# Performance work log

Measured on AMD Instinct MI355X. Metric: run time of the kernel, lower is better.

## Reference

```python
import jax, jax.numpy as jnp
import numpy as np
import math

B, P = 64, 2048
E_DRUG, E_PATH = 512, 512
ATTN_DIM, H, DEPTH = 1024, 8, 1
HD = ATTN_DIM // (2 * H)          # head_dim = 64
SCALING = HD ** (-0.5)
LAMBDA_INIT = 0.8 - 0.6 * math.exp(-0.3 * DEPTH)
EPS_SM = 1e-20
EPS_RMS = 1e-5


def stable_softmax(x, eps=EPS_SM):
    x = x.astype(jnp.float32)
    x = x - jnp.max(x, axis=-1, keepdims=True)
    ex = jnp.exp(x)
    return ex / (jnp.sum(ex, axis=-1, keepdims=True) + eps)


def setup_inputs() -> dict:
    key = jax.random.key(0)
    ks = jax.random.split(key, 11)
    d = 2 * H * HD  # = ATTN_DIM
    return {
        "query": jax.random.normal(ks[0], (B, 1, E_DRUG), jnp.float32),
        "key": jax.random.normal(ks[1], (B, P, E_PATH), jnp.float32),
        # Linear weights stored [in, out] (transpose of torch storage; same math)
        "Wq": jax.random.normal(ks[2], (E_DRUG, d), jnp.float32) * 0.02,
        "Wk": jax.random.normal(ks[3], (E_PATH, d), jnp.float32) * 0.02,
        "Wv": jax.random.normal(ks[4], (E_PATH, d), jnp.float32) * 0.02,
        "Wo": jax.random.normal(ks[5], (d, E_DRUG), jnp.float32) * 0.02,
        "lambda_q1": jax.random.normal(ks[6], (HD,), jnp.float32) * 0.1,
        "lambda_k1": jax.random.normal(ks[7], (HD,), jnp.float32) * 0.1,
        "lambda_q2": jax.random.normal(ks[8], (HD,), jnp.float32) * 0.1,
        "lambda_k2": jax.random.normal(ks[9], (HD,), jnp.float32) * 0.1,
        "rms_weight": jnp.ones((2 * HD,), jnp.float32),
    }


def reference(query, key, Wq, Wk, Wv, Wo,
              lambda_q1, lambda_k1, lambda_q2, lambda_k2, rms_weight):
    # Q: [B,1,H,2,HD] -> [B,H,2,1,HD]; K,V: [B,P,H,2,HD] -> [B,H,2,P,HD]
    Q = (query @ Wq).reshape(B, 1, H, 2, HD).transpose(0, 2, 3, 1, 4) * SCALING
    K = (key @ Wk).reshape(B, P, H, 2, HD).transpose(0, 2, 3, 1, 4)
    V = (key @ Wv).reshape(B, P, H, 2, HD)

    # scores: [B,H,2,1,P]
    scores = jnp.einsum('bhsqd,bhskd->bhsqk', Q, K)
    scores = stable_softmax(scores)

    lam1 = jnp.exp(jnp.sum(lambda_q1 * lambda_k1))
    lam2 = jnp.exp(jnp.sum(lambda_q2 * lambda_k2))
    lam = lam1 - lam2 + LAMBDA_INIT

    diff_attn = scores[:, :, 0] - lam * scores[:, :, 1]  # [B,H,1,P]

    V_cat = V.transpose(0, 2, 1, 3, 4).reshape(B, H, P, 2 * HD)  # [B,H,P,2HD]
    out = jnp.einsum('bhqp,bhpd->bhqd', diff_attn, V_cat)        # [B,H,1,2HD]

    # RMSNorm over last dim, affine
    var = jnp.mean(out * out, axis=-1, keepdims=True)
    out = out * jax.lax.rsqrt(var + EPS_RMS) * rms_weight
    out = out * (1.0 - LAMBDA_INIT)

    out = out.transpose(0, 2, 1, 3).reshape(B, 1, 2 * H * HD)
    out = out @ Wo  # [B,1,E_DRUG]
    return out, diff_attn
```

## Files before the change

kernel.cpp:

```cpp
#include <hip/hip_runtime.h>
#include <hip/hip_bf16.h>
#include <math.h>

#define B_ 64
#define P_ 2048
#define E_ 512
#define H_ 8
#define D_ 1024
#define NC_ 32
#define NG_ 4
#define SMEM_FUSED (65536 + 8704 + 2304 + 64 + 64)

#define BAR() do { asm volatile("s_waitcnt lgkmcnt(0)" ::: "memory"); \
                   __builtin_amdgcn_s_barrier(); } while (0)

static constexpr float SCALING_C = 0.125f;
static constexpr float LAMBDA_INIT_C = 0.35550906759096966f;

typedef float f32x4 __attribute__((ext_vector_type(4)));
typedef float f32x2 __attribute__((ext_vector_type(2)));
typedef short bf16x8 __attribute__((ext_vector_type(8)));

static __device__ __forceinline__ short f2bf(float f) {
    unsigned u = __builtin_bit_cast(unsigned, f);
    unsigned r = (u + 0x7fffu + ((u >> 16) & 1u)) >> 16;
    return (short)r;
}

__global__ __launch_bounds__(256) void k_qproj(const float* __restrict__ query,
                                               const float* __restrict__ Wq,
                                               const float* __restrict__ Wk,
                                               unsigned short* __restrict__ qkfrag) {
    int x = blockIdx.x, b = blockIdx.y, t = threadIdx.x;
    __shared__ float q[E_];
    __shared__ float qh[256];
    q[t] = query[b * E_ + t];
    q[t + 256] = query[b * E_ + t + 256];
    __syncthreads();
    {
        int j = x * 256 + t;
        const float* w = Wq + j;
        float s0 = 0.f, s1 = 0.f, s2 = 0.f, s3 = 0.f;
        #pragma unroll 4
        for (int e = 0; e < E_; e += 4) {
            s0 += q[e]     * w[(long)e * D_];
            s1 += q[e + 1] * w[(long)(e + 1) * D_];
            s2 += q[e + 2] * w[(long)(e + 2) * D_];
            s3 += q[e + 3] * w[(long)(e + 3) * D_];
        }
        qh[t] = ((s0 + s1) + (s2 + s3)) * SCALING_C;
    }
    __syncthreads();
    int hs_loc = t >> 6, l = t & 63;
    int hs = x * 4 + hs_loc;
    int e0 = l * 8;
    const float* qp = qh + hs_loc * 64;
    float acc[8];
    #pragma unroll
    for (int jj = 0; jj < 8; ++jj) {
        const f32x4* w = (const f32x4*)(Wk + (long)(e0 + jj) * D_ + hs * 64);
        float s = 0.f;
        #pragma unroll
        for (int d4 = 0; d4 < 16; ++d4) {
            f32x4 wv = w[d4];
            s += qp[d4 * 4 + 0] * wv[0] + qp[d4 * 4 + 1] * wv[1]
               + qp[d4 * 4 + 2] * wv[2] + qp[d4 * 4 + 3] * wv[3];
        }
        acc[jj] = s;
    }
    bf16x8 v;
    #pragma unroll
    for (int jj = 0; jj < 8; ++jj) v[jj] = f2bf(acc[jj]);
    *(bf16x8*)(qkfrag + (((long)b * 16 + (l >> 2)) * 64 + (l & 3) * 16 + hs) * 8) = v;
}

__global__ __launch_bounds__(512, 2) void k_fusedp(const float* __restrict__ key,
                                                   const unsigned short* __restrict__ qkfrag,
                                                   float* __restrict__ wexp,
                                                   float* __restrict__ ms, float* __restrict__ zs,
                                                   float* __restrict__ apart) {
    extern __shared__ __align__(16) char smem[];
    unsigned short* kswz = (unsigned short*)smem;
    float* scr           = (float*)(smem + 65536);
    unsigned short* wbf  = (unsigned short*)(smem + 74240);
    float* fac_l         = (float*)(smem + 76544);
    float* mrun_l        = (float*)(smem + 76608);

    int pcg = blockIdx.x, b = blockIdx.y;
    int t = threadIdx.x, wv = t >> 6, l = t & 63;
    int rt = wv >> 1, eh = wv & 1;
    int prow = rt * 16 + (l & 15);
    int xorv = ((prow & 7) << 3) ^ ((prow & 8) << 1);
    int ebase = eh * 256 + (l >> 4) * 8;

    if (t < 16) mrun_l[t] = -3.0e38f;

    bf16x8 qfr[8];
    {
        const bf16x8* qf = (const bf16x8*)(qkfrag + (long)b * 16 * 64 * 8);
        #pragma unroll
        for (int s = 0; s < 8; ++s) qfr[s] = qf[(eh * 8 + s) * 64 + l];
    }

    const float* kp = key + ((long)b * P_ + pcg * 512 + prow) * E_ + ebase;

    f32x4 x[16];
    #pragma unroll
    for (int s = 0; s < 8; ++s) {
        x[2 * s]     = *(const f32x4*)(kp + s * 32);
        x[2 * s + 1] = *(const f32x4*)(kp + s * 32 + 4);
    }

    f32x4 accp[4];
    #pragma unroll
    for (int i = 0; i < 4; ++i) accp[i] = {0.f, 0.f, 0.f, 0.f};

    for (int c = 0; c < 8; ++c) {
        {
            f32x4 acc = {0.f, 0.f, 0.f, 0.f};
            #pragma unroll
            for (int s = 0; s < 8; ++s) {
                f32x4 x0 = x[2 * s], x1 = x[2 * s + 1];
                bf16x8 a;
                a[0] = f2bf(x0[0]); a[1] = f2bf(x0[1]); a[2] = f2bf(x0[2]); a[3] = f2bf(x0[3]);
                a[4] = f2bf(x1[0]); a[5] = f2bf(x1[1]); a[6] = f2bf(x1[2]); a[7] = f2bf(x1[3]);
                *(bf16x8*)(kswz + prow * 512 + ((ebase + s * 32) ^ xorv)) = a;
                acc = __builtin_amdgcn_mfma_f32_16x16x32_bf16(a, qfr[s], acc, 0, 0, 0);
            }
            #pragma unroll
            for (int r = 0; r < 4; ++r)
                scr[eh * 1088 + (l & 15) * 68 + rt * 16 + (l >> 4) * 4 + r] = acc[r];
        }
        if (c < 7) {
            const float* kpn = kp + (long)(c + 1) * 64 * E_;
            #pragma unroll
            for (int s = 0; s < 8; ++s) {
                x[2 * s]     = *(const f32x4*)(kpn + s * 32);
                x[2 * s + 1] = *(const f32x4*)(kpn + s * 32 + 4);
            }
        }
        BAR();

        {
            int hs = t >> 5, i = t & 31;
            const float* s0p = scr + hs * 68 + i * 2;
            const float* s1p = s0p + 1088;
            float v0 = s0p[0] + s1p[0];
            float v1 = s0p[1] + s1p[1];
            float m = fmaxf(v0, v1);
            #pragma unroll
            for (int o = 16; o > 0; o >>= 1) m = fmaxf(m, __shfl_xor(m, o));
            float e0v = expf(v0 - m), e1v = expf(v1 - m);
            float z = e0v + e1v;
            #pragma unroll
            for (int o = 16; o > 0; o >>= 1) z += __shfl_xor(z, o);
            float mold = mrun_l[hs];
            float mnew = fmaxf(mold, m);
            float wsc = expf(m - mnew);
            if (i == 0) {
                mrun_l[hs] = mnew;
                fac_l[hs] = expf(mold - mnew);
                ms[((long)(pcg * 8 + c) * B_ + b) * 16 + hs] = m;
                zs[((long)(pcg * 8 + c) * B_ + b) * 16 + hs] = z;
            }
            f32x2 wv2; wv2[0] = e0v; wv2[1] = e1v;
            *(f32x2*)(wexp + ((long)b * 16 + hs) * P_ + pcg * 512 + c * 64 + i * 2) = wv2;
            unsigned lo = (unsigned short)f2bf(e0v * wsc);
            unsigned hi = (unsigned short)f2bf(e1v * wsc);
            *(unsigned*)(wbf + hs * 72 + i * 2) = lo | (hi << 16);
        }
        BAR();

        {
            f32x4 frv;
            frv[0] = fac_l[(l >> 4) * 4 + 0];
            frv[1] = fac_l[(l >> 4) * 4 + 1];
            frv[2] = fac_l[(l >> 4) * 4 + 2];
            frv[3] = fac_l[(l >> 4) * 4 + 3];
            const unsigned short* wrow = wbf + (l & 15) * 72;
            #pragma unroll
            for (int tile = 0; tile < 4; ++tile) {
                accp[tile] = accp[tile] * frv;
                int e = wv * 64 + tile * 16 + (l & 15);
                #pragma unroll
                for (int ks = 0; ks < 2; ++ks) {
                    int pbase = ks * 32 + (l >> 4) * 8;
                    bf16x8 af = *(const bf16x8*)(wrow + pbase);
                    int x2 = (pbase & 8) << 1;
                    bf16x8 bfv;
                    #pragma unroll
                    for (int j = 0; j < 8; ++j)
                        bfv[j] = (short)kswz[(pbase + j) * 512 + (e ^ (j << 3) ^ x2)];
                    accp[tile] = __builtin_amdgcn_mfma_f32_16x16x32_bf16(af, bfv, accp[tile], 0, 0, 0);
                }
            }
        }
        BAR();
    }

    {
        long abase = ((long)pcg * B_ + b) * 16 * E_;
        #pragma unroll
        for (int tile = 0; tile < 4; ++tile) {
            int e = wv * 64 + tile * 16 + (l & 15);
            #pragma unroll
            for (int r = 0; r < 4; ++r)
                apart[abase + (long)((l >> 4) * 4 + r) * E_ + e] = accp[tile][r];
        }
    }
}

__global__ __launch_bounds__(256) void k_comb(const float* __restrict__ wexp,
                                              const float* __restrict__ ms, const float* __restrict__ zs,
                                              const float* __restrict__ apart,
                                              const float* __restrict__ lq1, const float* __restrict__ lk1,
                                              const float* __restrict__ lq2, const float* __restrict__ lk2,
                                              const float* __restrict__ Wv, const float* __restrict__ rmsw,
                                              float* __restrict__ out1, float* __restrict__ on) {
    int h = blockIdx.x, b = blockIdx.y, t = threadIdx.x;
    __shared__ float lam_s;
    __shared__ float mc0s[NC_], mc1s[NC_], zc0s[NC_], zc1s[NC_];
    __shared__ float c0s[NC_], c1s[NC_];
    __shared__ float attk[E_];
    __shared__ float onred[2][128];
    __shared__ float red[4];
    int hs0 = 2 * h, hs1 = 2 * h + 1;
    if (t < 64) {
        float v1 = lq1[t] * lk1[t];
        float v2 = lq2[t] * lk2[t];
        #pragma unroll
        for (int o = 32; o > 0; o >>= 1) { v1 += __shfl_xor(v1, o); v2 += __shfl_xor(v2, o); }
        if (t == 0) lam_s = expf(v1) - expf(v2) + LAMBDA_INIT_C;
    }
    if (t >= 64 && t < 64 + NC_) {
        int c = t - 64;
        mc0s[c] = ms[((long)c * B_ + b) * 16 + hs0];
        mc1s[c] = ms[((long)c * B_ + b) * 16 + hs1];
        zc0s[c] = zs[((long)c * B_ + b) * 16 + hs0];
        zc1s[c] = zs[((long)c * B_ + b) * 16 + hs1];
    }
    __syncthreads();
    float m0 = -3.0e38f, m1 = -3.0e38f;
    #pragma unroll
    for (int c = 0; c < NC_; ++c) { m0 = fmaxf(m0, mc0s[c]); m1 = fmaxf(m1, mc1s[c]); }
    float z0 = 0.f, z1 = 0.f;
    #pragma unroll
    for (int c = 0; c < NC_; ++c) {
        z0 += zc0s[c] * expf(mc0s[c] - m0);
        z1 += zc1s[c] * expf(mc1s[c] - m1);
    }
    float lam = lam_s;
    float i0 = 1.f / (z0 + 1e-20f);
    float i1 = lam / (z1 + 1e-20f);
    if (t < NC_) {
        c0s[t] = expf(mc0s[t] - m0) * i0;
        c1s[t] = expf(mc1s[t] - m1) * i1;
    }
    __syncthreads();
    const float* w0p = wexp + ((long)b * 16 + hs0) * P_;
    const float* w1p = wexp + ((long)b * 16 + hs1) * P_;
    float* dst = out1 + ((long)b * H_ + h) * P_;
    #pragma unroll
    for (int c8 = 0; c8 < 8; ++c8) {
        int p = c8 * 256 + t;
        dst[p] = w0p[p] * c0s[p >> 6] - w1p[p] * c1s[p >> 6];
    }
    float cg0[NG_], cg1[NG_];
    #pragma unroll
    for (int g = 0; g < NG_; ++g) {
        float mg0 = -3.0e38f, mg1 = -3.0e38f;
        #pragma unroll
        for (int q = 0; q < 8; ++q) {
            mg0 = fmaxf(mg0, mc0s[g * 8 + q]);
            mg1 = fmaxf(mg1, mc1s[g * 8 + q]);
        }
        cg0[g] = expf(mg0 - m0) * i0;
        cg1[g] = expf(mg1 - m1) * i1;
    }
    #pragma unroll
    for (int k = 0; k < 2; ++k) {
        int e = k * 256 + t;
        float s = 0.f;
        #pragma unroll
        for (int g = 0; g < NG_; ++g) {
            s += cg0[g] * apart[(((long)g * B_ + b) * 16 + hs0) * E_ + e]
               - cg1[g] * apart[(((long)g * B_ + b) * 16 + hs1) * E_ + e];
        }
        attk[e] = s;
    }
    __syncthreads();
    int j = t & 127, half = t >> 7;
    const float* w = Wv + (long)(half * 256) * D_ + h * 128 + j;
    const float* aa = attk + half * 256;
    float s0 = 0.f, s1 = 0.f, s2 = 0.f, s3 = 0.f;
    #pragma unroll 8
    for (int e = 0; e < 256; e += 4) {
        s0 += aa[e]     * w[(long)e * D_];
        s1 += aa[e + 1] * w[(long)(e + 1) * D_];
        s2 += aa[e + 2] * w[(long)(e + 2) * D_];
        s3 += aa[e + 3] * w[(long)(e + 3) * D_];
    }
    onred[half][j] = (s0 + s1) + (s2 + s3);
    __syncthreads();
    float v = 0.f;
    if (t < 128) v = onred[0][t] + onred[1][t];
    float sq = v * v;
    int wv2 = t >> 6, ln = t & 63;
    #pragma unroll
    for (int o = 32; o > 0; o >>= 1) sq += __shfl_xor(sq, o);
    if (ln == 0) red[wv2] = sq;
    __syncthreads();
    float tot = red[0] + red[1];
    float scale = rsqrtf(tot * (1.f / 128.f) + 1e-5f) * (1.f - LAMBDA_INIT_C);
    if (t < 128) on[(long)b * D_ + h * 128 + t] = v * scale * rmsw[t];
}

__global__ __launch_bounds__(256) void k_wo(const float* __restrict__ on,
                                            const float* __restrict__ Wo,
                                            float* __restrict__ wop) {
    int kc = blockIdx.x >> 1, oc = blockIdx.x & 1, b = blockIdx.y;
    int t = threadIdx.x;
    __shared__ float sh[256];
    sh[t] = on[(long)b * D_ + kc * 256 + t];
    __syncthreads();
    int o = oc * 256 + t;
    const float* w = Wo + (long)(kc * 256) * 512 + o;
    float s0 = 0.f, s1 = 0.f, s2 = 0.f, s3 = 0.f;
    #pragma unroll 8
    for (int k = 0; k < 256; k += 4) {
        s0 += sh[k]     * w[(long)k * 512];
        s1 += sh[k + 1] * w[(long)(k + 1) * 512];
        s2 += sh[k + 2] * w[(long)(k + 2) * 512];
        s3 += sh[k + 3] * w[(long)(k + 3) * 512];
    }
    wop[((long)kc * B_ + b) * 512 + o] = (s0 + s1) + (s2 + s3);
}

__global__ __launch_bounds__(256) void k_wored(const float* __restrict__ wop,
                                               float* __restrict__ out0) {
    int b = blockIdx.x, t = threadIdx.x;
    #pragma unroll
    for (int i = 0; i < 2; ++i) {
        int o = i * 256 + t;
        float s = 0.f;
        #pragma unroll
        for (int kc = 0; kc < 4; ++kc) s += wop[((long)kc * B_ + b) * 512 + o];
        out0[(long)b * 512 + o] = s;
    }
}

extern "C" void kernel_launch(void* const* d_in, const int* in_sizes, int n_in,
                              void* d_out, int out_size, void* d_ws, size_t ws_size,
                              hipStream_t stream) {
    const float* query = (const float*)d_in[0];
    const float* key   = (const float*)d_in[1];
    const float* Wq    = (const float*)d_in[2];
    const float* Wk    = (const float*)d_in[3];
    const float* Wv    = (const float*)d_in[4];
    const float* Wo    = (const float*)d_in[5];
    const float* lq1   = (const float*)d_in[6];
    const float* lk1   = (const float*)d_in[7];
    const float* lq2   = (const float*)d_in[8];
    const float* lk2   = (const float*)d_in[9];
    const float* rmsw  = (const float*)d_in[10];

    float* out0 = (float*)d_out;
    float* out1 = out0 + B_ * E_;

    unsigned short* qkfrag = (unsigned short*)d_ws;
    float* wexp  = (float*)d_ws + 262144;
    float* apart = wexp + (long)B_ * 16 * P_;
    float* ms    = apart + (long)NG_ * B_ * 16 * E_;
    float* zs    = ms + NC_ * B_ * 16;
    float* on    = zs + NC_ * B_ * 16;
    float* wop   = on + B_ * D_;

    hipFuncSetAttribute((const void*)k_fusedp,
                        hipFuncAttributeMaxDynamicSharedMemorySize, SMEM_FUSED);

    hipLaunchKernelGGL(k_qproj,  dim3(4, B_),   dim3(256), 0, stream, query, Wq, Wk, qkfrag);
    hipLaunchKernelGGL(k_fusedp, dim3(NG_, B_), dim3(512), SMEM_FUSED, stream,
                       key, qkfrag, wexp, ms, zs, apart);
    hipLaunchKernelGGL(k_comb,   dim3(H_, B_),  dim3(256), 0, stream, wexp, ms, zs, apart,
                       lq1, lk1, lq2, lk2, Wv, rmsw, out1, on);
    hipLaunchKernelGGL(k_wo,     dim3(8, B_),   dim3(256), 0, stream, on, Wo, wop);
    hipLaunchKernelGGL(k_wored,  dim3(B_),      dim3(256), 0, stream, wop, out0);
}
```

Baseline: 123.6 us.

## Coalesce key loads in fused kernel and widen GEMV accumulators to eight

```diff
diff --git a/kernel.cpp b/kernel.cpp
--- a/kernel.cpp
+++ b/kernel.cpp
@@ -20,6 +20,7 @@
 typedef float f32x4 __attribute__((ext_vector_type(4)));
 typedef float f32x2 __attribute__((ext_vector_type(2)));
 typedef short bf16x8 __attribute__((ext_vector_type(8)));
+typedef short bf16x4 __attribute__((ext_vector_type(4)));
 
 static __device__ __forceinline__ short f2bf(float f) {
     unsigned u = __builtin_bit_cast(unsigned, f);
@@ -40,15 +41,13 @@
     {
         int j = x * 256 + t;
         const float* w = Wq + j;
-        float s0 = 0.f, s1 = 0.f, s2 = 0.f, s3 = 0.f;
+        float s[8] = {0.f,0.f,0.f,0.f,0.f,0.f,0.f,0.f};
         #pragma unroll 4
-        for (int e = 0; e < E_; e += 4) {
-            s0 += q[e]     * w[(long)e * D_];
-            s1 += q[e + 1] * w[(long)(e + 1) * D_];
-            s2 += q[e + 2] * w[(long)(e + 2) * D_];
-            s3 += q[e + 3] * w[(long)(e + 3) * D_];
-        }
-        qh[t] = ((s0 + s1) + (s2 + s3)) * SCALING_C;
+        for (int e = 0; e < E_; e += 8) {
+            #pragma unroll
+            for (int k = 0; k < 8; ++k) s[k] += q[e + k] * w[(long)(e + k) * D_];
+        }
+        qh[t] = (((s[0]+s[1])+(s[2]+s[3])) + ((s[4]+s[5])+(s[6]+s[7]))) * SCALING_C;
     }
     __syncthreads();
     int hs_loc = t >> 6, l = t & 63;
@@ -91,7 +90,8 @@
     int rt = wv >> 1, eh = wv & 1;
     int prow = rt * 16 + (l & 15);
     int xorv = ((prow & 7) << 3) ^ ((prow & 8) << 1);
-    int ebase = eh * 256 + (l >> 4) * 8;
+    int hi = t >> 7;
+    int col4 = t & 127;
 
     if (t < 16) mrun_l[t] = -3.0e38f;
 
@@ -102,42 +102,46 @@
         for (int s = 0; s < 8; ++s) qfr[s] = qf[(eh * 8 + s) * 64 + l];
     }
 
-    const float* kp = key + ((long)b * P_ + pcg * 512 + prow) * E_ + ebase;
+    const float* kchunk = key + ((long)b * P_ + pcg * 512) * E_;
 
     f32x4 x[16];
     #pragma unroll
-    for (int s = 0; s < 8; ++s) {
-        x[2 * s]     = *(const f32x4*)(kp + s * 32);
-        x[2 * s + 1] = *(const f32x4*)(kp + s * 32 + 4);
-    }
+    for (int r = 0; r < 16; ++r)
+        x[r] = *(const f32x4*)(kchunk + (long)(r * 512 + t) * 4);
 
     f32x4 accp[4];
     #pragma unroll
     for (int i = 0; i < 4; ++i) accp[i] = {0.f, 0.f, 0.f, 0.f};
 
     for (int c = 0; c < 8; ++c) {
+        #pragma unroll
+        for (int r = 0; r < 16; ++r) {
+            int row = 4 * r + hi;
+            int xr = ((row & 7) << 3) ^ ((row & 8) << 1);
+            bf16x4 wb;
+            wb[0] = f2bf(x[r][0]); wb[1] = f2bf(x[r][1]);
+            wb[2] = f2bf(x[r][2]); wb[3] = f2bf(x[r][3]);
+            *(bf16x4*)(kswz + row * 512 + ((col4 * 4) ^ xr)) = wb;
+        }
+        if (c < 7) {
+            const float* kn = kchunk + (long)(c + 1) * 64 * E_;
+            #pragma unroll
+            for (int r = 0; r < 16; ++r)
+                x[r] = *(const f32x4*)(kn + (long)(r * 512 + t) * 4);
+        }
+        BAR();
+
         {
             f32x4 acc = {0.f, 0.f, 0.f, 0.f};
             #pragma unroll
             for (int s = 0; s < 8; ++s) {
-                f32x4 x0 = x[2 * s], x1 = x[2 * s + 1];
-                bf16x8 a;
-                a[0] = f2bf(x0[0]); a[1] = f2bf(x0[1]); a[2] = f2bf(x0[2]); a[3] = f2bf(x0[3]);
-                a[4] = f2bf(x1[0]); a[5] = f2bf(x1[1]); a[6] = f2bf(x1[2]); a[7] = f2bf(x1[3]);
-                *(bf16x8*)(kswz + prow * 512 + ((ebase + s * 32) ^ xorv)) = a;
+                int e8 = eh * 256 + (l >> 4) * 8 + s * 32;
+                bf16x8 a = *(const bf16x8*)(kswz + prow * 512 + (e8 ^ xorv));
                 acc = __builtin_amdgcn_mfma_f32_16x16x32_bf16(a, qfr[s], acc, 0, 0, 0);
             }
             #pragma unroll
             for (int r = 0; r < 4; ++r)
                 scr[eh * 1088 + (l & 15) * 68 + rt * 16 + (l >> 4) * 4 + r] = acc[r];
-        }
-        if (c < 7) {
-            const float* kpn = kp + (long)(c + 1) * 64 * E_;
-            #pragma unroll
-            for (int s = 0; s < 8; ++s) {
-                x[2 * s]     = *(const f32x4*)(kpn + s * 32);
-                x[2 * s + 1] = *(const f32x4*)(kpn + s * 32 + 4);
-            }
         }
         BAR();
 
@@ -166,8 +170,8 @@
             f32x2 wv2; wv2[0] = e0v; wv2[1] = e1v;
             *(f32x2*)(wexp + ((long)b * 16 + hs) * P_ + pcg * 512 + c * 64 + i * 2) = wv2;
             unsigned lo = (unsigned short)f2bf(e0v * wsc);
-            unsigned hi = (unsigned short)f2bf(e1v * wsc);
-            *(unsigned*)(wbf + hs * 72 + i * 2) = lo | (hi << 16);
+            unsigned hi2 = (unsigned short)f2bf(e1v * wsc);
+            *(unsigned*)(wbf + hs * 72 + i * 2) = lo | (hi2 << 16);
         }
         BAR();
 
@@ -292,15 +296,13 @@
     int j = t & 127, half = t >> 7;
     const float* w = Wv + (long)(half * 256) * D_ + h * 128 + j;
     const float* aa = attk + half * 256;
-    float s0 = 0.f, s1 = 0.f, s2 = 0.f, s3 = 0.f;
-    #pragma unroll 8
-    for (int e = 0; e < 256; e += 4) {
-        s0 += aa[e]     * w[(long)e * D_];
-        s1 += aa[e + 1] * w[(long)(e + 1) * D_];
-        s2 += aa[e + 2] * w[(long)(e + 2) * D_];
-        s3 += aa[e + 3] * w[(long)(e + 3) * D_];
-    }
-    onred[half][j] = (s0 + s1) + (s2 + s3);
+    float s[8] = {0.f,0.f,0.f,0.f,0.f,0.f,0.f,0.f};
+    #pragma unroll 4
+    for (int e = 0; e < 256; e += 8) {
+        #pragma unroll
+        for (int k = 0; k < 8; ++k) s[k] += aa[e + k] * w[(long)(e + k) * D_];
+    }
+    onred[half][j] = ((s[0]+s[1])+(s[2]+s[3])) + ((s[4]+s[5])+(s[6]+s[7]));
     __syncthreads();
     float v = 0.f;
     if (t < 128) v = onred[0][t] + onred[1][t];
@@ -325,15 +327,13 @@
     __syncthreads();
     int o = oc * 256 + t;
     const float* w = Wo + (long)(kc * 256) * 512 + o;
-    float s0 = 0.f, s1 = 0.f, s2 = 0.f, s3 = 0.f;
-    #pragma unroll 8
-    for (int k = 0; k < 256; k += 4) {
-        s0 += sh[k]     * w[(long)k * 512];
-        s1 += sh[k + 1] * w[(long)(k + 1) * 512];
-        s2 += sh[k + 2] * w[(long)(k + 2) * 512];
-        s3 += sh[k + 3] * w[(long)(k + 3) * 512];
-    }
-    wop[((long)kc * B_ + b) * 512 + o] = (s0 + s1) + (s2 + s3);
+    float s[8] = {0.f,0.f,0.f,0.f,0.f,0.f,0.f,0.f};
+    #pragma unroll 4
+    for (int k = 0; k < 256; k += 8) {
+        #pragma unroll
+        for (int q = 0; q < 8; ++q) s[q] += sh[k + q] * w[(long)(k + q) * 512];
+    }
+    wop[((long)kc * B_ + b) * 512 + o] = ((s[0]+s[1])+(s[2]+s[3])) + ((s[4]+s[5])+(s[6]+s[7]));
 }
 
 __global__ __launch_bounds__(256) void k_wored(const float* __restrict__ wop,
```

Measured after the change: 121.1 us. -2.0%, faster.
